# Optimization experiments

Measured on AMD Instinct MI355X. Metric: run time of the kernel, lower is better.

Reference implementation:

```python
import jax, jax.numpy as jnp
import numpy as np

N_NODES = 50000
N_EDGES = 800000
D_IN = 128
D_HID = 512
D_OUT = 128


def setup_inputs() -> dict:
    key = jax.random.key(0)
    k1, k2, k3, k4, k5, k6 = jax.random.split(key, 6)
    input_matrix = jax.random.normal(k1, (N_NODES, D_IN), dtype=jnp.float32)
    adjacency_coo_matrix = jax.random.randint(k2, (2, N_EDGES), 0, N_NODES, dtype=jnp.int64)
    # fc net params (torch Linear: y = x @ W.T + b); store W already transposed [D_IN, D_HID]
    lim_fc = 1.0 / np.sqrt(D_IN)
    fc_w = jax.random.uniform(k3, (D_IN, D_HID), dtype=jnp.float32, minval=-lim_fc, maxval=lim_fc)
    fc_b = jax.random.uniform(k4, (D_HID,), dtype=jnp.float32, minval=-lim_fc, maxval=lim_fc)
    # xavier_uniform for [D_IN + D_HID, D_OUT]
    lim_w = np.sqrt(6.0 / (D_IN + D_HID + D_OUT))
    weights_matrix = jax.random.uniform(k5, (D_IN + D_HID, D_OUT), dtype=jnp.float32, minval=-lim_w, maxval=lim_w)
    return {
        "input_matrix": input_matrix,
        "fc_w": fc_w,
        "fc_b": fc_b,
        "weights_matrix": weights_matrix,
        "adjacency_coo_matrix": adjacency_coo_matrix,
    }


def reference(input_matrix, fc_w, fc_b, weights_matrix, adjacency_coo_matrix):
    edge_src, edge_trg = adjacency_coo_matrix[0], adjacency_coo_matrix[1]
    n_nodes = input_matrix.shape[0]
    # gather neighbor features: [E, D_IN]
    neighbors = input_matrix[edge_trg]
    # per-edge MLP + relu: [E, D_HID]
    neighbors_repr = jax.nn.relu(neighbors @ fc_w + fc_b)
    # scatter-max reduce into per-node slots; relu outputs are >= 0, and
    # empty segments map to 0 (matching torch_scatter zero-fill), so clamp at 0
    agg = jax.ops.segment_max(neighbors_repr, edge_src, num_segments=n_nodes)
    agg = jnp.maximum(agg, 0.0)
    concat = jnp.concatenate([input_matrix, agg], axis=1)  # [N, D_IN + D_HID]
    return concat @ weights_matrix  # [N, D_OUT]
```

## Files before the change

### kernel.cpp

```cpp
#include <hip/hip_runtime.h>
#include <hip/hip_bf16.h>

#define N_NODES 50000
#define N_EDGES 800000
#define D_IN 128
#define D_HID 512
#define D_OUT 128
#define CAT_DIM 640
#define CAP 64

typedef __attribute__((ext_vector_type(8))) short short8;
typedef __attribute__((ext_vector_type(4))) float floatx4;

__device__ __forceinline__ unsigned short f2bf(float f) {
    unsigned u = __float_as_uint(f);
    unsigned r = u + 0x7fffu + ((u >> 16) & 1u);
    return (unsigned short)(r >> 16);
}


#define PREP_CASTX_BLOCKS   6250
#define PREP_FCW_BLOCKS      256
#define PREP_W2_BLOCKS       320
#define PREP_DEG_BLOCKS      196
#define PREP_TOTAL_BLOCKS  (PREP_CASTX_BLOCKS + PREP_FCW_BLOCKS + PREP_W2_BLOCKS + PREP_DEG_BLOCKS + 1)

__global__ void prep_kernel(const float* __restrict__ X, const float* __restrict__ fcW,
                            const float* __restrict__ Wm, const int* __restrict__ adj,
                            unsigned short* __restrict__ concat,
                            unsigned short* __restrict__ fcwT,
                            unsigned short* __restrict__ WT,
                            int* __restrict__ deg, int* __restrict__ flag) {
    int b = blockIdx.x;
    int tid = threadIdx.x;
    if (b < PREP_CASTX_BLOCKS) {
        int t = b * 256 + tid;
        int row = t >> 5;
        int cg2 = (t & 31) * 4;
        float4 v = *(const float4*)(X + (size_t)row * D_IN + cg2);
        unsigned short o[4] = { f2bf(v.x), f2bf(v.y), f2bf(v.z), f2bf(v.w) };
        *(unsigned long long*)(concat + (size_t)row * CAT_DIM + cg2) = *(unsigned long long*)o;
        return;
    }
    b -= PREP_CASTX_BLOCKS;
    if (b < PREP_FCW_BLOCKS) {
        int idx = b * 256 + tid;
        int k = idx >> 9;
        int n = idx & (D_HID - 1);
        fcwT[n * D_IN + k] = f2bf(fcW[idx]);
        return;
    }
    b -= PREP_FCW_BLOCKS;
    if (b < PREP_W2_BLOCKS) {
        int idx = b * 256 + tid;
        int k = idx >> 7;
        int n = idx & (D_OUT - 1);
        WT[n * CAT_DIM + k] = f2bf(Wm[idx]);
        return;
    }
    b -= PREP_W2_BLOCKS;
    if (b < PREP_DEG_BLOCKS) {
        int idx = b * 256 + tid;
        if (idx < N_NODES) deg[idx] = 0;
        return;
    }
    if (tid < 64) {
        int v = adj[2 * tid + 1];
        unsigned long long m = __ballot(v != 0);
        if (tid == 0) *flag = (m == 0ULL) ? 2 : 1;
    }
}


__device__ __forceinline__ void hist_edges(const int* __restrict__ adj, int s, int e0,
                                           int* __restrict__ deg, int* __restrict__ edge_list) {
    int src0, src1, trg0, trg1;
    if (s == 2) {
        int4 vs = *(const int4*)(adj + 2 * (size_t)e0);
        int4 vt = *(const int4*)(adj + 2 * ((size_t)N_EDGES + e0));
        src0 = vs.x; src1 = vs.z;
        trg0 = vt.x; trg1 = vt.z;
    } else {
        int2 vs = *(const int2*)(adj + e0);
        int2 vt = *(const int2*)(adj + N_EDGES + e0);
        src0 = vs.x; src1 = vs.y;
        trg0 = vt.x; trg1 = vt.y;
    }
    int p0 = atomicAdd(&deg[src0], 1);
    if (p0 < CAP) edge_list[src0 * CAP + p0] = trg0;
    int p1 = atomicAdd(&deg[src1], 1);
    if (p1 < CAP) edge_list[src1 * CAP + p1] = trg1;
}


#define GPAD 8
#define SM64_BYTES ((64 + 128) * (64 + GPAD) * 2)

template<int BIAS_RELU, int OUT_BF16>
__device__ __forceinline__ void gemm_tile64(char* smem,
    const unsigned short* __restrict__ A, int lda,
    const unsigned short* __restrict__ Bt, int ldb,
    const float* __restrict__ bias, void* __restrict__ Cout, int ldc,
    int M, int K, int bm, int bn)
{
    constexpr int BK = 64;
    typedef unsigned short Row[BK + GPAD];
    Row* As = (Row*)smem;
    Row* Bs = (Row*)(smem + 64 * (BK + GPAD) * 2);
    int tid = threadIdx.x;
    int lane = tid & 63, w = tid >> 6;
    int wm = (w >> 1) * 32, wn = (w & 1) * 64;
    int q = lane >> 4, l16 = lane & 15;
    floatx4 acc[2][4] = {};
    int ra = tid >> 2;
    int ca = (tid & 3) * 8;
    int rb = tid >> 1;
    int cb = (tid & 1) * 8;

    for (int k0 = 0; k0 < K; k0 += BK) {
        {
            int gr = bm + ra;
            const unsigned short* ap = A + (size_t)gr * lda + k0 + ca;
            #pragma unroll
            for (int p = 0; p < 2; ++p) {
                uint4 va = make_uint4(0u, 0u, 0u, 0u);
                if (gr < M) va = *(const uint4*)(ap + p * 32);
                *(uint4*)(&As[ra][ca + p * 32]) = va;
            }
        }
        {
            const unsigned short* bp = Bt + (size_t)(bn + rb) * ldb + k0 + cb;
            #pragma unroll
            for (int p = 0; p < 4; ++p)
                *(uint4*)(&Bs[rb][cb + p * 16]) = *(const uint4*)(bp + p * 16);
        }
        __syncthreads();
        #pragma unroll
        for (int ks = 0; ks < 2; ++ks) {
            short8 af[2], bf[4];
            #pragma unroll
            for (int mi = 0; mi < 2; ++mi)
                af[mi] = *(const short8*)(&As[wm + mi * 16 + l16][ks * 32 + q * 8]);
            #pragma unroll
            for (int ni = 0; ni < 4; ++ni)
                bf[ni] = *(const short8*)(&Bs[wn + ni * 16 + l16][ks * 32 + q * 8]);
            #pragma unroll
            for (int mi = 0; mi < 2; ++mi)
                #pragma unroll
                for (int ni = 0; ni < 4; ++ni)
                    acc[mi][ni] = __builtin_amdgcn_mfma_f32_16x16x32_bf16(af[mi], bf[ni], acc[mi][ni], 0, 0, 0);
        }
        __syncthreads();
    }

    #pragma unroll
    for (int mi = 0; mi < 2; ++mi) {
        #pragma unroll
        for (int ni = 0; ni < 4; ++ni) {
            #pragma unroll
            for (int r = 0; r < 4; ++r) {
                int row = bm + wm + mi * 16 + q * 4 + r;
                int col = bn + wn + ni * 16 + l16;
                if (row < M) {
                    float v = acc[mi][ni][r];
                    if (BIAS_RELU) v = fmaxf(v + bias[col], 0.0f);
                    if (OUT_BF16) ((unsigned short*)Cout)[(size_t)row * ldc + col] = f2bf(v);
                    else          ((float*)Cout)[(size_t)row * ldc + col] = v;
                }
            }
        }
    }
}


#define HIST_VB     1563
#define GEMM1_MT     782
#define GEMM1_TILES (GEMM1_MT * 4)

__global__ __launch_bounds__(256)
void mid_kernel(const int* __restrict__ adj, const int* __restrict__ flag,
                int* __restrict__ deg, int* __restrict__ edge_list,
                const unsigned short* __restrict__ concat,
                const unsigned short* __restrict__ fcwT,
                const float* __restrict__ fcb,
                unsigned short* __restrict__ F) {
    if (blockIdx.x < HIST_VB) {
        int e0 = (blockIdx.x * 256 + threadIdx.x) * 2;
        if (e0 < N_EDGES) hist_edges(adj, flag[0], e0, deg, edge_list);
        return;
    }
    __shared__ char smem[SM64_BYTES];
    int tile = blockIdx.x - HIST_VB;
    gemm_tile64<1, 1>(smem, concat, CAT_DIM, fcwT, D_IN, fcb, F, D_HID,
                      N_NODES, D_IN, (tile >> 2) * 64, (tile & 3) * 128);
}


__device__ __forceinline__ void fmax_bf16x8(float* acc, const uint4& p) {
    const unsigned* a = (const unsigned*)&p;
    #pragma unroll
    for (int j = 0; j < 4; ++j) {
        unsigned u = a[j];
        acc[2 * j]     = fmaxf(acc[2 * j],     __uint_as_float(u << 16));
        acc[2 * j + 1] = fmaxf(acc[2 * j + 1], __uint_as_float(u & 0xffff0000u));
    }
}

__global__ __launch_bounds__(256)
void aggregate_kernel(const unsigned short* __restrict__ F,
                      const int* __restrict__ deg,
                      const int* __restrict__ edge_list,
                      unsigned short* __restrict__ concat) {
    int gw = (blockIdx.x * 256 + threadIdx.x) >> 6;
    if (gw >= N_NODES) return;
    int lane = threadIdx.x & 63;
    int d = deg[gw];
    d = d < CAP ? d : CAP;
    const int* el = edge_list + gw * CAP;
    float acc[8] = {0.f, 0.f, 0.f, 0.f, 0.f, 0.f, 0.f, 0.f};
    int i = 0;
    for (; i + 2 <= d; i += 2) {
        int t0 = el[i], t1 = el[i + 1];
        uint4 p0 = *(const uint4*)(F + (size_t)t0 * D_HID + lane * 8);
        uint4 p1 = *(const uint4*)(F + (size_t)t1 * D_HID + lane * 8);
        fmax_bf16x8(acc, p0);
        fmax_bf16x8(acc, p1);
    }
    if (i < d) {
        uint4 p0 = *(const uint4*)(F + (size_t)el[i] * D_HID + lane * 8);
        fmax_bf16x8(acc, p0);
    }
    unsigned out[4];
    #pragma unroll
    for (int j = 0; j < 4; ++j) {
        unsigned lo = __float_as_uint(acc[2 * j]) >> 16;
        unsigned hi = __float_as_uint(acc[2 * j + 1]) & 0xffff0000u;
        out[j] = lo | hi;
    }
    *(uint4*)(concat + (size_t)gw * CAT_DIM + D_IN + lane * 8) = *(uint4*)out;
}


__global__ __launch_bounds__(256)
void gemm2_kernel(const unsigned short* __restrict__ concat,
                  const unsigned short* __restrict__ WT,
                  float* __restrict__ out) {
    __shared__ char smem[SM64_BYTES];
    gemm_tile64<0, 0>(smem, concat, CAT_DIM, WT, CAT_DIM, nullptr, out, D_OUT,
                      N_NODES, CAT_DIM, blockIdx.x * 64, 0);
}


extern "C" void kernel_launch(void* const* d_in, const int* in_sizes, int n_in,
                              void* d_out, int out_size, void* d_ws, size_t ws_size,
                              hipStream_t stream) {
    const float* X    = (const float*)d_in[0];
    const float* fc_w = (const float*)d_in[1];
    const float* fc_b = (const float*)d_in[2];
    const float* Wm   = (const float*)d_in[3];
    const int*   adj  = (const int*)d_in[4];
    float* outp = (float*)d_out;

    char* ws = (char*)d_ws;
    size_t off = 0;
    auto alloc = [&](size_t bytes) -> void* {
        void* p = ws + off;
        off = (off + bytes + 255) & ~(size_t)255;
        return p;
    };
    unsigned short* concat = (unsigned short*)alloc((size_t)N_NODES * CAT_DIM * 2);
    unsigned short* F      = (unsigned short*)alloc((size_t)N_NODES * D_HID * 2);
    unsigned short* fcwT   = (unsigned short*)alloc((size_t)D_HID * D_IN * 2);
    unsigned short* WT     = (unsigned short*)alloc((size_t)D_OUT * CAT_DIM * 2);
    int* deg       = (int*)alloc((size_t)N_NODES * 4);
    int* edge_list = (int*)alloc((size_t)N_NODES * CAP * 4);
    int* flag      = (int*)alloc(256);

    prep_kernel<<<PREP_TOTAL_BLOCKS, 256, 0, stream>>>(X, fc_w, Wm, adj, concat, fcwT, WT, deg, flag);
    mid_kernel<<<HIST_VB + GEMM1_TILES, 256, 0, stream>>>(adj, flag, deg, edge_list,
                                                          concat, fcwT, fc_b, F);
    aggregate_kernel<<<(N_NODES * 64) / 256, 256, 0, stream>>>(F, deg, edge_list, concat);
    gemm2_kernel<<<GEMM1_MT, 256, 0, stream>>>(concat, WT, outp);
}
```

Before: 288.9 us.

## Fuse neighbor max-aggregation with the output GEMM in one kernel

Merges the aggregate and second GEMM kernels. Each block aggregates 16 nodes into the concat buffer, syncs, then computes those 16 output rows with MFMA, reading A and B fragments straight from global memory without LDS staging. The goal is to drop a kernel launch and read the freshly written concat rows while they are still cache-hot. The cost is a small 16-row tile per block with no shared-memory reuse of the weight matrix, which is reloaded from L2 by every block. The old GEMM helper is inlined into mid_kernel.

```diff
diff --git a/kernel.cpp b/kernel.cpp
--- a/kernel.cpp
+++ b/kernel.cpp
@@ -93,89 +93,11 @@
 }
 
 
-#define GPAD 8
-#define SM64_BYTES ((64 + 128) * (64 + GPAD) * 2)
-
-template<int BIAS_RELU, int OUT_BF16>
-__device__ __forceinline__ void gemm_tile64(char* smem,
-    const unsigned short* __restrict__ A, int lda,
-    const unsigned short* __restrict__ Bt, int ldb,
-    const float* __restrict__ bias, void* __restrict__ Cout, int ldc,
-    int M, int K, int bm, int bn)
-{
-    constexpr int BK = 64;
-    typedef unsigned short Row[BK + GPAD];
-    Row* As = (Row*)smem;
-    Row* Bs = (Row*)(smem + 64 * (BK + GPAD) * 2);
-    int tid = threadIdx.x;
-    int lane = tid & 63, w = tid >> 6;
-    int wm = (w >> 1) * 32, wn = (w & 1) * 64;
-    int q = lane >> 4, l16 = lane & 15;
-    floatx4 acc[2][4] = {};
-    int ra = tid >> 2;
-    int ca = (tid & 3) * 8;
-    int rb = tid >> 1;
-    int cb = (tid & 1) * 8;
-
-    for (int k0 = 0; k0 < K; k0 += BK) {
-        {
-            int gr = bm + ra;
-            const unsigned short* ap = A + (size_t)gr * lda + k0 + ca;
-            #pragma unroll
-            for (int p = 0; p < 2; ++p) {
-                uint4 va = make_uint4(0u, 0u, 0u, 0u);
-                if (gr < M) va = *(const uint4*)(ap + p * 32);
-                *(uint4*)(&As[ra][ca + p * 32]) = va;
-            }
-        }
-        {
-            const unsigned short* bp = Bt + (size_t)(bn + rb) * ldb + k0 + cb;
-            #pragma unroll
-            for (int p = 0; p < 4; ++p)
-                *(uint4*)(&Bs[rb][cb + p * 16]) = *(const uint4*)(bp + p * 16);
-        }
-        __syncthreads();
-        #pragma unroll
-        for (int ks = 0; ks < 2; ++ks) {
-            short8 af[2], bf[4];
-            #pragma unroll
-            for (int mi = 0; mi < 2; ++mi)
-                af[mi] = *(const short8*)(&As[wm + mi * 16 + l16][ks * 32 + q * 8]);
-            #pragma unroll
-            for (int ni = 0; ni < 4; ++ni)
-                bf[ni] = *(const short8*)(&Bs[wn + ni * 16 + l16][ks * 32 + q * 8]);
-            #pragma unroll
-            for (int mi = 0; mi < 2; ++mi)
-                #pragma unroll
-                for (int ni = 0; ni < 4; ++ni)
-                    acc[mi][ni] = __builtin_amdgcn_mfma_f32_16x16x32_bf16(af[mi], bf[ni], acc[mi][ni], 0, 0, 0);
-        }
-        __syncthreads();
-    }
-
-    #pragma unroll
-    for (int mi = 0; mi < 2; ++mi) {
-        #pragma unroll
-        for (int ni = 0; ni < 4; ++ni) {
-            #pragma unroll
-            for (int r = 0; r < 4; ++r) {
-                int row = bm + wm + mi * 16 + q * 4 + r;
-                int col = bn + wn + ni * 16 + l16;
-                if (row < M) {
-                    float v = acc[mi][ni][r];
-                    if (BIAS_RELU) v = fmaxf(v + bias[col], 0.0f);
-                    if (OUT_BF16) ((unsigned short*)Cout)[(size_t)row * ldc + col] = f2bf(v);
-                    else          ((float*)Cout)[(size_t)row * ldc + col] = v;
-                }
-            }
-        }
-    }
-}
-
-
 #define HIST_VB     1563
 #define GEMM1_MT     782
 #define GEMM1_TILES (GEMM1_MT * 4)
+#define GPAD 8
+#define SM64_BYTES ((64 + 128) * (64 + GPAD) * 2)
 
 __global__ __launch_bounds__(256)
 void mid_kernel(const int* __restrict__ adj, const int* __restrict__ flag,
@@ -189,12 +111,78 @@
         if (e0 < N_EDGES) hist_edges(adj, flag[0], e0, deg, edge_list);
         return;
     }
+    constexpr int BK = 64;
+    typedef unsigned short Row[BK + GPAD];
     __shared__ char smem[SM64_BYTES];
+    Row* As = (Row*)smem;
+    Row* Bs = (Row*)(smem + 64 * (BK + GPAD) * 2);
     int tile = blockIdx.x - HIST_VB;
-    gemm_tile64<1, 1>(smem, concat, CAT_DIM, fcwT, D_IN, fcb, F, D_HID,
-                      N_NODES, D_IN, (tile >> 2) * 64, (tile & 3) * 128);
-}
-
+    int bm = (tile >> 2) * 64, bn = (tile & 3) * 128;
+    int tid = threadIdx.x;
+    int lane = tid & 63, w = tid >> 6;
+    int wm = (w >> 1) * 32, wn = (w & 1) * 64;
+    int q = lane >> 4, l16 = lane & 15;
+    floatx4 acc[2][4] = {};
+    int ra = tid >> 2;
+    int ca = (tid & 3) * 8;
+    int rb = tid >> 1;
+    int cb = (tid & 1) * 8;
+
+    for (int k0 = 0; k0 < D_IN; k0 += BK) {
+        {
+            int gr = bm + ra;
+            const unsigned short* ap = concat + (size_t)gr * CAT_DIM + k0 + ca;
+            #pragma unroll
+            for (int p = 0; p < 2; ++p) {
+                uint4 va = make_uint4(0u, 0u, 0u, 0u);
+                if (gr < N_NODES) va = *(const uint4*)(ap + p * 32);
+                *(uint4*)(&As[ra][ca + p * 32]) = va;
+            }
+        }
+        {
+            const unsigned short* bp = fcwT + (size_t)(bn + rb) * D_IN + k0 + cb;
+            #pragma unroll
+            for (int p = 0; p < 4; ++p)
+                *(uint4*)(&Bs[rb][cb + p * 16]) = *(const uint4*)(bp + p * 16);
+        }
+        __syncthreads();
+        #pragma unroll
+        for (int ks = 0; ks < 2; ++ks) {
+            short8 af[2], bf[4];
+            #pragma unroll
+            for (int mi = 0; mi < 2; ++mi)
+                af[mi] = *(const short8*)(&As[wm + mi * 16 + l16][ks * 32 + q * 8]);
+            #pragma unroll
+            for (int ni = 0; ni < 4; ++ni)
+                bf[ni] = *(const short8*)(&Bs[wn + ni * 16 + l16][ks * 32 + q * 8]);
+            #pragma unroll
+            for (int mi = 0; mi < 2; ++mi)
+                #pragma unroll
+                for (int ni = 0; ni < 4; ++ni)
+                    acc[mi][ni] = __builtin_amdgcn_mfma_f32_16x16x32_bf16(af[mi], bf[ni], acc[mi][ni], 0, 0, 0);
+        }
+        __syncthreads();
+    }
+
+    #pragma unroll
+    for (int mi = 0; mi < 2; ++mi) {
+        #pragma unroll
+        for (int ni = 0; ni < 4; ++ni) {
+            #pragma unroll
+            for (int r = 0; r < 4; ++r) {
+                int row = bm + wm + mi * 16 + q * 4 + r;
+                int col = bn + wn + ni * 16 + l16;
+                if (row < N_NODES) {
+                    float v = fmaxf(acc[mi][ni][r] + fcb[col], 0.0f);
+                    F[(size_t)row * D_HID + col] = f2bf(v);
+                }
+            }
+        }
+    }
+}
+
+
+#define AGF_BLOCKS 3125
 
 __device__ __forceinline__ void fmax_bf16x8(float* acc, const uint4& p) {
     const unsigned* a = (const unsigned*)&p;
@@ -207,47 +195,68 @@
 }
 
 __global__ __launch_bounds__(256)
-void aggregate_kernel(const unsigned short* __restrict__ F,
-                      const int* __restrict__ deg,
-                      const int* __restrict__ edge_list,
-                      unsigned short* __restrict__ concat) {
-    int gw = (blockIdx.x * 256 + threadIdx.x) >> 6;
-    if (gw >= N_NODES) return;
-    int lane = threadIdx.x & 63;
-    int d = deg[gw];
-    d = d < CAP ? d : CAP;
-    const int* el = edge_list + gw * CAP;
-    float acc[8] = {0.f, 0.f, 0.f, 0.f, 0.f, 0.f, 0.f, 0.f};
-    int i = 0;
-    for (; i + 2 <= d; i += 2) {
-        int t0 = el[i], t1 = el[i + 1];
-        uint4 p0 = *(const uint4*)(F + (size_t)t0 * D_HID + lane * 8);
-        uint4 p1 = *(const uint4*)(F + (size_t)t1 * D_HID + lane * 8);
-        fmax_bf16x8(acc, p0);
-        fmax_bf16x8(acc, p1);
-    }
-    if (i < d) {
-        uint4 p0 = *(const uint4*)(F + (size_t)el[i] * D_HID + lane * 8);
-        fmax_bf16x8(acc, p0);
-    }
-    unsigned out[4];
-    #pragma unroll
-    for (int j = 0; j < 4; ++j) {
-        unsigned lo = __float_as_uint(acc[2 * j]) >> 16;
-        unsigned hi = __float_as_uint(acc[2 * j + 1]) & 0xffff0000u;
-        out[j] = lo | hi;
-    }
-    *(uint4*)(concat + (size_t)gw * CAT_DIM + D_IN + lane * 8) = *(uint4*)out;
-}
-
-
-__global__ __launch_bounds__(256)
-void gemm2_kernel(const unsigned short* __restrict__ concat,
-                  const unsigned short* __restrict__ WT,
-                  float* __restrict__ out) {
-    __shared__ char smem[SM64_BYTES];
-    gemm_tile64<0, 0>(smem, concat, CAT_DIM, WT, CAT_DIM, nullptr, out, D_OUT,
-                      N_NODES, CAT_DIM, blockIdx.x * 64, 0);
+void aggfull_kernel(const unsigned short* __restrict__ F,
+                    const int* __restrict__ deg,
+                    const int* __restrict__ edge_list,
+                    unsigned short* __restrict__ concat,
+                    const unsigned short* __restrict__ WT,
+                    float* __restrict__ out) {
+    int tid = threadIdx.x;
+    int lane = tid & 63, wv = tid >> 6;
+    int bm = blockIdx.x * 16;
+
+    #pragma unroll
+    for (int nn = 0; nn < 4; ++nn) {
+        int node = bm + wv * 4 + nn;
+        int d = deg[node];
+        d = d < CAP ? d : CAP;
+        const int* el = edge_list + node * CAP;
+        float acc[8] = {0.f, 0.f, 0.f, 0.f, 0.f, 0.f, 0.f, 0.f};
+        int i = 0;
+        for (; i + 2 <= d; i += 2) {
+            int t0 = el[i], t1 = el[i + 1];
+            uint4 p0 = *(const uint4*)(F + (size_t)t0 * D_HID + lane * 8);
+            uint4 p1 = *(const uint4*)(F + (size_t)t1 * D_HID + lane * 8);
+            fmax_bf16x8(acc, p0);
+            fmax_bf16x8(acc, p1);
+        }
+        if (i < d) {
+            uint4 p0 = *(const uint4*)(F + (size_t)el[i] * D_HID + lane * 8);
+            fmax_bf16x8(acc, p0);
+        }
+        unsigned o[4];
+        #pragma unroll
+        for (int j = 0; j < 4; ++j) {
+            unsigned lo = __float_as_uint(acc[2 * j]) >> 16;
+            unsigned hi = __float_as_uint(acc[2 * j + 1]) & 0xffff0000u;
+            o[j] = lo | hi;
+        }
+        *(uint4*)(concat + (size_t)node * CAT_DIM + D_IN + lane * 8) = *(uint4*)o;
+    }
+    __syncthreads();
+
+    int q = lane >> 4, l16 = lane & 15;
+    floatx4 acc2[2] = {};
+    const unsigned short* arow = concat + (size_t)(bm + l16) * CAT_DIM + q * 8;
+    const unsigned short* b0 = WT + (size_t)(wv * 32 + l16) * CAT_DIM + q * 8;
+    const unsigned short* b1 = b0 + (size_t)16 * CAT_DIM;
+    #pragma unroll
+    for (int k0 = 0; k0 < CAT_DIM; k0 += 32) {
+        short8 af  = *(const short8*)(arow + k0);
+        short8 bf0 = *(const short8*)(b0 + k0);
+        short8 bf1 = *(const short8*)(b1 + k0);
+        acc2[0] = __builtin_amdgcn_mfma_f32_16x16x32_bf16(af, bf0, acc2[0], 0, 0, 0);
+        acc2[1] = __builtin_amdgcn_mfma_f32_16x16x32_bf16(af, bf1, acc2[1], 0, 0, 0);
+    }
+    #pragma unroll
+    for (int ni = 0; ni < 2; ++ni) {
+        #pragma unroll
+        for (int r = 0; r < 4; ++r) {
+            int row = bm + q * 4 + r;
+            int col = wv * 32 + ni * 16 + l16;
+            out[(size_t)row * D_OUT + col] = acc2[ni][r];
+        }
+    }
 }
 
 
@@ -279,6 +288,5 @@
     prep_kernel<<<PREP_TOTAL_BLOCKS, 256, 0, stream>>>(X, fc_w, Wm, adj, concat, fcwT, WT, deg, flag);
     mid_kernel<<<HIST_VB + GEMM1_TILES, 256, 0, stream>>>(adj, flag, deg, edge_list,
                                                           concat, fcwT, fc_b, F);
-    aggregate_kernel<<<(N_NODES * 64) / 256, 256, 0, stream>>>(F, deg, edge_list, concat);
-    gemm2_kernel<<<GEMM1_MT, 256, 0, stream>>>(concat, WT, outp);
-}
+    aggfull_kernel<<<AGF_BLOCKS, 256, 0, stream>>>(F, deg, edge_list, concat, WT, outp);
+}
```

Measured after the change: 358.4 us. 24.1% more time.
